# Performance work log

Hardware: AMD Instinct MI355X
Metric: run time of the kernel (lower is better)

The kernel has to match this reference:

```python
import jax, jax.numpy as jnp
import numpy as np

NUM_HEADS = 16
D_MODEL = 1024
D_K = D_MODEL // NUM_HEADS
MAX_SEQ_LEN = 4096
ROPE_BASE = 10000.0
BATCH = 2
SEQ_LEN = 2048


def _rope_tables(seq_len, d_k, base=ROPE_BASE):
    # theta_i = 1 / base^(2i/d_k), i = 0..d_k/2-1
    theta = 1.0 / base ** (jnp.arange(0, d_k, 2, dtype=jnp.float32) / d_k)
    m = jnp.arange(seq_len, dtype=jnp.float32)
    m_theta = jnp.outer(m, theta)                      # [S, d_k/2]
    ang = jnp.concatenate([m_theta, m_theta], axis=-1)  # [S, d_k]
    return jnp.cos(ang), jnp.sin(ang)


def _apply_rope(x, cos, sin):
    # x: [B, H, S, d_k]; rotate-half: cat(-x2, x1)
    d2 = x.shape[-1] // 2
    x1, x2 = x[..., :d2], x[..., d2:]
    x_flip = jnp.concatenate([-x2, x1], axis=-1)
    return x * cos + x_flip * sin


def setup_inputs() -> dict:
    key = jax.random.key(0)
    kx, kq, kk, kv, ko = jax.random.split(key, 5)
    s = 1.0 / np.sqrt(D_MODEL)  # ~ nn.Linear default init scale
    x = jax.random.normal(kx, (BATCH, SEQ_LEN, D_MODEL), dtype=jnp.float32)
    W_Q = jax.random.uniform(kq, (D_MODEL, D_MODEL), jnp.float32, -s, s)
    W_K = jax.random.uniform(kk, (D_MODEL, D_MODEL), jnp.float32, -s, s)
    W_V = jax.random.uniform(kv, (D_MODEL, D_MODEL), jnp.float32, -s, s)
    W_O = jax.random.uniform(ko, (D_MODEL, D_MODEL), jnp.float32, -s, s)
    return {"x": x, "W_Q": W_Q, "W_K": W_K, "W_V": W_V, "W_O": W_O}


def reference(x, W_Q, W_K, W_V, W_O):
    B, S, _ = x.shape
    # Linear with weight [out, in]: y = x @ W.T
    def proj(W):
        y = jnp.einsum('bsd,ed->bse', x, W)
        return y.reshape(B, S, NUM_HEADS, D_K).transpose(0, 2, 1, 3)  # [B,H,S,dk]
    Q, K, V = proj(W_Q), proj(W_K), proj(W_V)
    cos, sin = _rope_tables(S, D_K)
    Q = _apply_rope(Q, cos, sin)
    K = _apply_rope(K, cos, sin)
    scores = jnp.einsum('bhsd,bhtd->bhst', Q, K) / jnp.sqrt(jnp.float32(D_K))
    causal = jnp.tril(jnp.ones((S, S), dtype=bool))
    scores = jnp.where(causal[None, None], scores, -jnp.inf)
    attn = jax.nn.softmax(scores, axis=-1)
    out = jnp.einsum('bhst,bhtd->bhsd', attn, V)
    out = out.transpose(0, 2, 1, 3).reshape(B, S, D_MODEL)
    return jnp.einsum('bsd,ed->bse', out, W_O)
```

## Files before the change

kernel.cpp:

```cpp
#include <hip/hip_runtime.h>
#include <hip/hip_bf16.h>

#define BATCH 2
#define SEQ 2048
#define DM 1024
#define NH 16
#define DKH 64

typedef __attribute__((ext_vector_type(8))) __bf16 bf16x8;
typedef __attribute__((ext_vector_type(4))) float f32x4;
typedef __attribute__((ext_vector_type(2))) float f32x2;
typedef __attribute__((ext_vector_type(8))) unsigned short ushort8;

__device__ __forceinline__ void gload16(const void* g, void* l) {
  __builtin_amdgcn_global_load_lds(
      (const __attribute__((address_space(1))) void*)g,
      (__attribute__((address_space(3))) void*)l, 16, 0, 0);
}

__global__ void cast_x(const float* __restrict__ in, __bf16* __restrict__ out) {
  int i = blockIdx.x * blockDim.x + threadIdx.x;
  f32x4 a = ((const f32x4*)in)[2 * i], b = ((const f32x4*)in)[2 * i + 1];
  bf16x8 o;
  o[0]=(__bf16)a[0]; o[1]=(__bf16)a[1]; o[2]=(__bf16)a[2]; o[3]=(__bf16)a[3];
  o[4]=(__bf16)b[0]; o[5]=(__bf16)b[1]; o[6]=(__bf16)b[2]; o[7]=(__bf16)b[3];
  ((bf16x8*)out)[i] = o;
}

__global__ void cast_w(const float* __restrict__ w0, const float* __restrict__ w1,
                       const float* __restrict__ w2, const float* __restrict__ w3,
                       __bf16* __restrict__ out) {
  const float* src = (blockIdx.y == 0) ? w0 : (blockIdx.y == 1) ? w1
                   : (blockIdx.y == 2) ? w2 : w3;
  __bf16* dst = out + (size_t)blockIdx.y * (DM * DM);
  int i = blockIdx.x * blockDim.x + threadIdx.x;
  f32x4 a = ((const f32x4*)src)[2 * i], b = ((const f32x4*)src)[2 * i + 1];
  bf16x8 o;
  o[0]=(__bf16)a[0]; o[1]=(__bf16)a[1]; o[2]=(__bf16)a[2]; o[3]=(__bf16)a[3];
  o[4]=(__bf16)b[0]; o[5]=(__bf16)b[1]; o[6]=(__bf16)b[2]; o[7]=(__bf16)b[3];
  ((bf16x8*)dst)[i] = o;
}

__global__ void gen_tab(float* __restrict__ tab) {
  int idx = blockIdx.x * blockDim.x + threadIdx.x;
  int s = idx >> 5, i = idx & 31;
  float theta = exp2f((float)i * -0.41524101186092029f);
  float sn, c;
  sincosf((float)s * theta, &sn, &c);
  tab[2 * idx] = c;
  tab[2 * idx + 1] = sn;
}

#define QSCALE 0.1803368801111137f

template<int EPI, int BN>
__launch_bounds__(256, 3)
__global__ void gemm_bt(const __bf16* __restrict__ A, const __bf16* __restrict__ B,
                        void* __restrict__ Cout, int M, int N, int K,
                        const float* __restrict__ tab) {
  __shared__ __bf16 As[128 * 64];
  __shared__ __bf16 Bs[BN * 64];
  const int tid = threadIdx.x;
  const int lane = tid & 63;
  const int w = tid >> 6;
  const int wr = w >> 1, wc = w & 1;
  const int fr = lane & 15, fq = lane >> 4;
  const int m0 = blockIdx.x * 128;
  const int n0 = blockIdx.y * BN;
  const int NFR = BN / 32;

  f32x4 acc[4][BN / 32] = {};
  const int NT = K >> 6;

  for (int kt = 0; kt < NT; ++kt) {
    const int k0 = kt << 6;
    __syncthreads();
    #pragma unroll
    for (int p = 0; p < 4; ++p) {
      int c = p * 256 + tid;
      int row = c >> 3, cs = (c & 7) ^ (row & 7);
      gload16(&A[(size_t)(m0 + row) * K + k0 + cs * 8], &As[(p * 256 + w * 64) * 8]);
    }
    #pragma unroll
    for (int p = 0; p < BN / 32; ++p) {
      int c = p * 256 + tid;
      int row = c >> 3, cs = (c & 7) ^ (row & 7);
      gload16(&B[(size_t)(n0 + row) * K + k0 + cs * 8], &Bs[(p * 256 + w * 64) * 8]);
    }
    __syncthreads();
    #pragma unroll
    for (int kk = 0; kk < 2; ++kk) {
      bf16x8 af[4], bfr[BN / 32];
      #pragma unroll
      for (int mf = 0; mf < 4; ++mf) {
        int row = wr * 64 + mf * 16 + fr;
        af[mf] = *(const bf16x8*)&As[row * 64 + ((kk * 32 + fq * 8) ^ ((fr & 7) << 3))];
      }
      #pragma unroll
      for (int nf = 0; nf < NFR; ++nf) {
        int row = wc * (BN / 2) + nf * 16 + fr;
        bfr[nf] = *(const bf16x8*)&Bs[row * 64 + ((kk * 32 + fq * 8) ^ ((fr & 7) << 3))];
      }
      __builtin_amdgcn_s_setprio(1);
      #pragma unroll
      for (int mf = 0; mf < 4; ++mf)
        #pragma unroll
        for (int nf = 0; nf < NFR; ++nf)
          acc[mf][nf] = __builtin_amdgcn_mfma_f32_16x16x32_bf16(af[mf], bfr[nf], acc[mf][nf], 0, 0, 0);
      __builtin_amdgcn_s_setprio(0);
    }
  }

  if (EPI == 0) {
    const int nbase = n0 + wc * 64;
    const int which = nbase >> 10;
    const int h = (nbase & 1023) >> 6;
    const int b = m0 >> 11;
    __bf16* base0 = (__bf16*)Cout + (size_t)which * (4u << 20);
    if (which < 2) {
      const float scale = (which == 0) ? QSCALE : 1.0f;
      __bf16* dst = base0 + ((size_t)(b * NH + h)) * SEQ * DKH;
      #pragma unroll
      for (int mf = 0; mf < 4; ++mf) {
        #pragma unroll
        for (int j = 0; j < 4; ++j) {
          int s = (m0 & (SEQ - 1)) + wr * 64 + mf * 16 + fq * 4 + j;
          #pragma unroll
          for (int nf = 0; nf < 2; ++nf) {
            int i = nf * 16 + fr;
            f32x2 cs = ((const f32x2*)tab)[s * 32 + i];
            float a = acc[mf][nf][j], bb = acc[mf][nf + 2][j];
            dst[(size_t)s * DKH + i]      = (__bf16)((a * cs[0] - bb * cs[1]) * scale);
            dst[(size_t)s * DKH + i + 32] = (__bf16)((bb * cs[0] + a * cs[1]) * scale);
          }
        }
      }
    } else {
      __bf16* dst = base0 + ((size_t)(b * NH + h)) * DKH * SEQ;
      #pragma unroll
      for (int mf = 0; mf < 4; ++mf) {
        #pragma unroll
        for (int nf = 0; nf < 4; ++nf) {
          int dk = nf * 16 + fr;
          #pragma unroll
          for (int j = 0; j < 4; ++j) {
            int s = (m0 & (SEQ - 1)) + wr * 64 + mf * 16 + fq * 4 + j;
            dst[(size_t)dk * SEQ + s] = (__bf16)acc[mf][nf][j];
          }
        }
      }
    }
  } else {
    #pragma unroll
    for (int mf = 0; mf < 4; ++mf)
      #pragma unroll
      for (int nf = 0; nf < NFR; ++nf)
        #pragma unroll
        for (int j = 0; j < 4; ++j) {
          int m = m0 + wr * 64 + mf * 16 + fq * 4 + j;
          int n = n0 + wc * (BN / 2) + nf * 16 + fr;
          ((float*)Cout)[(size_t)m * N + n] = acc[mf][nf][j];
        }
  }
}

__launch_bounds__(512, 4)
__global__ void attn_causal(const __bf16* __restrict__ Qg, const __bf16* __restrict__ Kg,
                            const __bf16* __restrict__ Vtg, __bf16* __restrict__ Out) {
  __shared__ __bf16 Ks[2][64 * 64];
  __shared__ __bf16 Vts[2][64 * 64];
  __shared__ __bf16 Pl[8][16 * 64];
  const int tid = threadIdx.x;
  const int lane = tid & 63;
  const int w = tid >> 6;
  const int fr = lane & 15, fq = lane >> 4;
  const int bid = blockIdx.x;
  const int z = bid >> 8;
  const int r = bid & 255;
  const int c = (r >> 1) & 15;
  const int p = r & 1;
  const int hh = r >> 5;
  const int qa = (z ^ p) ? (15 - c) : c;
  const int h = hh | (p << 3);
  const int b = z;
  const int qb = 31 - qa;
  const int myqt = (w >> 2) ? qb : qa;
  const int q0 = myqt * 64;
  const int qrow_lo = q0 + (w & 3) * 16;
  const size_t bh = (size_t)(b * NH + h);
  const __bf16* Qh = Qg + bh * SEQ * DKH;
  const __bf16* Kh = Kg + bh * SEQ * DKH;
  const __bf16* Vth = Vtg + bh * DKH * SEQ;

  bf16x8 qf[2];
  #pragma unroll
  for (int kk = 0; kk < 2; ++kk)
    qf[kk] = *(const bf16x8*)&Qh[(size_t)(qrow_lo + fr) * DKH + kk * 32 + fq * 8];

  f32x4 Oa[4] = {};
  float lsum[4] = {0.f, 0.f, 0.f, 0.f};

  const int nt = qb + 1;

  {
    int cch = w * 64 + lane;
    int row = cch >> 3, cs = (cch & 7) ^ (row & 7);
    gload16(&Kh[(size_t)row * DKH + cs * 8], &Ks[0][(w * 64) * 8]);
    gload16(&Vth[(size_t)row * SEQ + cs * 8], &Vts[0][(w * 64) * 8]);
  }
  __syncthreads();

  for (int it = 0; it < nt; ++it) {
    const int cur = it & 1;
    const int ts = it << 6;
    if (it + 1 < nt) {
      const int tn = ts + 64;
      int cch = w * 64 + lane;
      int row = cch >> 3, cs = (cch & 7) ^ (row & 7);
      gload16(&Kh[(size_t)(tn + row) * DKH + cs * 8], &Ks[cur ^ 1][(w * 64) * 8]);
      gload16(&Vth[(size_t)row * SEQ + tn + cs * 8], &Vts[cur ^ 1][(w * 64) * 8]);
    }
    if (ts <= qrow_lo + 15) {
      f32x4 sacc[4] = {};
      __builtin_amdgcn_s_setprio(1);
      #pragma unroll
      for (int kk = 0; kk < 2; ++kk) {
        #pragma unroll
        for (int nf = 0; nf < 4; ++nf) {
          int krow = nf * 16 + fr;
          bf16x8 kf = *(const bf16x8*)&Ks[cur][krow * 64 + ((kk * 32 + fq * 8) ^ ((fr & 7) << 3))];
          sacc[nf] = __builtin_amdgcn_mfma_f32_16x16x32_bf16(qf[kk], kf, sacc[nf], 0, 0, 0);
        }
      }
      __builtin_amdgcn_s_setprio(0);
      const bool need_mask = (ts + 63 > qrow_lo);
      #pragma unroll
      for (int nf = 0; nf < 4; ++nf) {
        #pragma unroll
        for (int j = 0; j < 4; ++j) {
          float v = sacc[nf][j];
          if (need_mask) {
            int qr = qrow_lo + fq * 4 + j;
            int tc = ts + nf * 16 + fr;
            if (tc > qr) v = -INFINITY;
          }
          float pv = exp2f(v);
          lsum[j] += pv;
          int row = fq * 4 + j;
          Pl[w][row * 64 + ((nf * 16 + fr) ^ ((row & 7) << 3))] = (__bf16)pv;
        }
      }
      __builtin_amdgcn_s_setprio(1);
      #pragma unroll
      for (int kk = 0; kk < 2; ++kk) {
        bf16x8 pa = *(const bf16x8*)&Pl[w][fr * 64 + ((kk * 32 + fq * 8) ^ ((fr & 7) << 3))];
        #pragma unroll
        for (int nf = 0; nf < 4; ++nf) {
          int d = nf * 16 + fr;
          bf16x8 vf = *(const bf16x8*)&Vts[cur][d * 64 + ((kk * 32 + fq * 8) ^ ((fr & 7) << 3))];
          Oa[nf] = __builtin_amdgcn_mfma_f32_16x16x32_bf16(pa, vf, Oa[nf], 0, 0, 0);
        }
      }
      __builtin_amdgcn_s_setprio(0);
    }
    __syncthreads();
  }
  float rl[4];
  #pragma unroll
  for (int j = 0; j < 4; ++j) {
    #pragma unroll
    for (int msk = 1; msk < 16; msk <<= 1)
      lsum[j] += __shfl_xor(lsum[j], msk);
    rl[j] = 1.0f / lsum[j];
  }
  #pragma unroll
  for (int nf = 0; nf < 4; ++nf) {
    #pragma unroll
    for (int j = 0; j < 4; ++j) {
      int qr = qrow_lo + fq * 4 + j;
      Out[((size_t)(b * SEQ) + qr) * DM + h * DKH + nf * 16 + fr] = (__bf16)(Oa[nf][j] * rl[j]);
    }
  }
}

extern "C" void kernel_launch(void* const* d_in, const int* in_sizes, int n_in,
                              void* d_out, int out_size, void* d_ws, size_t ws_size,
                              hipStream_t stream) {
  const float* x  = (const float*)d_in[0];
  const float* Wq = (const float*)d_in[1];
  const float* Wk = (const float*)d_in[2];
  const float* Wv = (const float*)d_in[3];
  const float* Wo = (const float*)d_in[4];

  char* ws = (char*)d_ws;
  __bf16* xb  = (__bf16*)(ws);
  __bf16* wqb = (__bf16*)(ws + ( 8u << 20));
  __bf16* wob = (__bf16*)(ws + (14u << 20));
  __bf16* Qb  = (__bf16*)(ws + (16u << 20));
  __bf16* Kb  = (__bf16*)(ws + (24u << 20));
  __bf16* Vtb = (__bf16*)(ws + (32u << 20));
  __bf16* Ab  = (__bf16*)(ws + (40u << 20));
  float*  tab = (float*)(ws + (48u << 20));

  cast_x<<<dim3(2048), dim3(256), 0, stream>>>(x, xb);
  cast_w<<<dim3(512, 4), dim3(256), 0, stream>>>(Wq, Wk, Wv, Wo, wqb);
  gen_tab<<<dim3(256), dim3(256), 0, stream>>>(tab);

  gemm_bt<0, 128><<<dim3(32, 24), dim3(256), 0, stream>>>(xb, wqb, Qb, BATCH * SEQ, 3 * DM, DM, tab);

  attn_causal<<<dim3(512), dim3(512), 0, stream>>>(Qb, Kb, Vtb, Ab);

  gemm_bt<1, 64><<<dim3(32, 16), dim3(256), 0, stream>>>(Ab, wob, d_out, BATCH * SEQ, DM, DM, nullptr);
}
```

Baseline: 115.7 us.

## Keep P in registers by computing S transposed and permuting V columns

The QK^T MFMA now takes its operands swapped, so each lane holds score elements laid out the way the PV MFMA expects its A operand. The probabilities are packed straight into bf16 registers, removing the per-wave LDS staging buffer for P along with its writes and reads. To make the keys line up, the projection kernel stores V-transpose with a permuted sequence order inside each 32-column group. The row-sum reduction becomes one scalar per lane plus a cross-lane shuffle, and launch bounds are raised to allow more resident blocks, which risks register pressure.

New measurement: 113.5 us. Within noise of the previous version (-1.9%).

```diff
diff --git a/kernel.cpp b/kernel.cpp
--- a/kernel.cpp
+++ b/kernel.cpp
@@ -144,8 +144,8 @@
           int dk = nf * 16 + fr;
           #pragma unroll
           for (int j = 0; j < 4; ++j) {
-            int s = (m0 & (SEQ - 1)) + wr * 64 + mf * 16 + fq * 4 + j;
-            dst[(size_t)dk * SEQ + s] = (__bf16)acc[mf][nf][j];
+            int sp = (m0 & (SEQ - 1)) + wr * 64 + (mf >> 1) * 32 + fq * 8 + (mf & 1) * 4 + j;
+            dst[(size_t)dk * SEQ + sp] = (__bf16)acc[mf][nf][j];
           }
         }
       }
@@ -164,12 +164,11 @@
   }
 }
 
-__launch_bounds__(512, 4)
+__launch_bounds__(512, 8)
 __global__ void attn_causal(const __bf16* __restrict__ Qg, const __bf16* __restrict__ Kg,
                             const __bf16* __restrict__ Vtg, __bf16* __restrict__ Out) {
   __shared__ __bf16 Ks[2][64 * 64];
   __shared__ __bf16 Vts[2][64 * 64];
-  __shared__ __bf16 Pl[8][16 * 64];
   const int tid = threadIdx.x;
   const int lane = tid & 63;
   const int w = tid >> 6;
@@ -198,7 +197,7 @@
     qf[kk] = *(const bf16x8*)&Qh[(size_t)(qrow_lo + fr) * DKH + kk * 32 + fq * 8];
 
   f32x4 Oa[4] = {};
-  float lsum[4] = {0.f, 0.f, 0.f, 0.f};
+  float lsum = 0.f;
 
   const int nt = qb + 1;
 
@@ -229,50 +228,52 @@
         for (int nf = 0; nf < 4; ++nf) {
           int krow = nf * 16 + fr;
           bf16x8 kf = *(const bf16x8*)&Ks[cur][krow * 64 + ((kk * 32 + fq * 8) ^ ((fr & 7) << 3))];
-          sacc[nf] = __builtin_amdgcn_mfma_f32_16x16x32_bf16(qf[kk], kf, sacc[nf], 0, 0, 0);
+          sacc[nf] = __builtin_amdgcn_mfma_f32_16x16x32_bf16(kf, qf[kk], sacc[nf], 0, 0, 0);
         }
       }
       __builtin_amdgcn_s_setprio(0);
       const bool need_mask = (ts + 63 > qrow_lo);
+      const int qr = qrow_lo + fr;
       #pragma unroll
       for (int nf = 0; nf < 4; ++nf) {
         #pragma unroll
         for (int j = 0; j < 4; ++j) {
           float v = sacc[nf][j];
           if (need_mask) {
-            int qr = qrow_lo + fq * 4 + j;
-            int tc = ts + nf * 16 + fr;
+            int tc = ts + nf * 16 + fq * 4 + j;
             if (tc > qr) v = -INFINITY;
           }
           float pv = exp2f(v);
-          lsum[j] += pv;
-          int row = fq * 4 + j;
-          Pl[w][row * 64 + ((nf * 16 + fr) ^ ((row & 7) << 3))] = (__bf16)pv;
-        }
-      }
+          lsum += pv;
+          sacc[nf][j] = pv;
+        }
+      }
+      bf16x8 pa[2];
+      #pragma unroll
+      for (int kk = 0; kk < 2; ++kk)
+        #pragma unroll
+        for (int e = 0; e < 8; ++e)
+          pa[kk][e] = (__bf16)sacc[2 * kk + (e >> 2)][e & 3];
       __builtin_amdgcn_s_setprio(1);
       #pragma unroll
       for (int kk = 0; kk < 2; ++kk) {
-        bf16x8 pa = *(const bf16x8*)&Pl[w][fr * 64 + ((kk * 32 + fq * 8) ^ ((fr & 7) << 3))];
         #pragma unroll
         for (int nf = 0; nf < 4; ++nf) {
           int d = nf * 16 + fr;
           bf16x8 vf = *(const bf16x8*)&Vts[cur][d * 64 + ((kk * 32 + fq * 8) ^ ((fr & 7) << 3))];
-          Oa[nf] = __builtin_amdgcn_mfma_f32_16x16x32_bf16(pa, vf, Oa[nf], 0, 0, 0);
+          Oa[nf] = __builtin_amdgcn_mfma_f32_16x16x32_bf16(pa[kk], vf, Oa[nf], 0, 0, 0);
         }
       }
       __builtin_amdgcn_s_setprio(0);
     }
     __syncthreads();
   }
+  lsum += __shfl_xor(lsum, 16);
+  lsum += __shfl_xor(lsum, 32);
   float rl[4];
   #pragma unroll
-  for (int j = 0; j < 4; ++j) {
-    #pragma unroll
-    for (int msk = 1; msk < 16; msk <<= 1)
-      lsum[j] += __shfl_xor(lsum[j], msk);
-    rl[j] = 1.0f / lsum[j];
-  }
+  for (int j = 0; j < 4; ++j)
+    rl[j] = 1.0f / __shfl(lsum, fq * 4 + j);
   #pragma unroll
   for (int nf = 0; nf < 4; ++nf) {
     #pragma unroll
```
